# Performance work log

Hardware: AMD Instinct MI355X
Metric: run time of the kernel (lower is better)

## Reference

```python
import jax, jax.numpy as jnp
import numpy as np

B, T, D, H, L = 65536, 8, 60, 128, 64


def _lstm_layer(x, Wih, Whh, bih, bhh):
    """Single LSTM layer, batch_first. x: [B,T,Din]. Returns (ys [B,T,H], h_last [B,H]).
    PyTorch gate order: i, f, g, o."""
    Bsz = x.shape[0]
    Hd = Whh.shape[1]
    # Precompute input contribution for all timesteps: [B,T,4H]
    xg = jnp.einsum('btd,gd->btg', x, Wih) + bih + bhh

    def step(carry, xt):
        h, c = carry
        g = xt + h @ Whh.T  # [B,4H]
        i, f, gg, o = jnp.split(g, 4, axis=-1)
        i = jax.nn.sigmoid(i)
        f = jax.nn.sigmoid(f)
        gg = jnp.tanh(gg)
        o = jax.nn.sigmoid(o)
        c = f * c + i * gg
        h = o * jnp.tanh(c)
        return (h, c), h

    h0 = jnp.zeros((Bsz, Hd), x.dtype)
    c0 = jnp.zeros((Bsz, Hd), x.dtype)
    (h_last, _), ys = jax.lax.scan(step, (h0, c0), jnp.swapaxes(xg, 0, 1))
    return jnp.swapaxes(ys, 0, 1), h_last


def setup_inputs() -> dict:
    key = jax.random.key(0)
    ks = jax.random.split(key, 24)
    s = 1.0 / np.sqrt(H)  # torch LSTM/Linear default uniform bound

    def u(k, shape):
        return jax.random.uniform(k, shape, jnp.float32, -s, s)

    inp = {"x": jax.random.normal(ks[0], (B, T, D), jnp.float32)}
    # encoder layer 0 (in=D), layer 1 (in=H); decoder layer 0 (in=L), layer 1 (in=H)
    dims = {"enc0": D, "enc1": H, "dec0": L, "dec1": H}
    i = 1
    for name, din in dims.items():
        inp[name + "_Wih"] = u(ks[i], (4 * H, din)); i += 1
        inp[name + "_Whh"] = u(ks[i], (4 * H, H)); i += 1
        inp[name + "_bih"] = u(ks[i], (4 * H,)); i += 1
        inp[name + "_bhh"] = u(ks[i], (4 * H,)); i += 1
    inp["W_lat"] = u(ks[i], (L, H)); i += 1
    inp["b_lat"] = u(ks[i], (L,)); i += 1
    inp["W_out"] = jax.random.uniform(ks[i], (D, H), jnp.float32, -s, s); i += 1
    inp["b_out"] = jax.random.uniform(ks[i], (D,), jnp.float32, -s, s)
    return inp


def reference(x,
              enc0_Wih, enc0_Whh, enc0_bih, enc0_bhh,
              enc1_Wih, enc1_Whh, enc1_bih, enc1_bhh,
              dec0_Wih, dec0_Whh, dec0_bih, dec0_bhh,
              dec1_Wih, dec1_Whh, dec1_bih, dec1_bhh,
              W_lat, b_lat, W_out, b_out):
    # Encoder (eval mode: inter-layer dropout is identity)
    h1, _ = _lstm_layer(x, enc0_Wih, enc0_Whh, enc0_bih, enc0_bhh)
    _, h_last = _lstm_layer(h1, enc1_Wih, enc1_Whh, enc1_bih, enc1_bhh)
    # Latent bottleneck from top-layer final hidden state
    z = h_last @ W_lat.T + b_lat  # [B,L]
    z_seq = jnp.broadcast_to(z[:, None, :], (z.shape[0], T, z.shape[1]))
    # Decoder
    d1, _ = _lstm_layer(z_seq, dec0_Wih, dec0_Whh, dec0_bih, dec0_bhh)
    d2, _ = _lstm_layer(d1, dec1_Wih, dec1_Whh, dec1_bih, dec1_bhh)
    recon = jnp.einsum('bth,dh->btd', d2, W_out) + b_out  # [B,T,D]
    return recon
```

## Files before the change

kernel.cpp:

```cpp
#include <hip/hip_runtime.h>

typedef _Float16 f16;
typedef _Float16 f16x8 __attribute__((ext_vector_type(8)));
typedef float    f32x4 __attribute__((ext_vector_type(4)));

#define MFMA16(a,b,c) __builtin_amdgcn_mfma_f32_16x16x32_f16(a,b,c,0,0,0)

#define HIST_S 1096
#define HB_S   136
#define HB_BUF 4352

__device__ __forceinline__ float sigm(float v){
  return __builtin_amdgcn_rcpf(1.f + __builtin_amdgcn_exp2f(-1.4426950408889634f*v));
}
__device__ __forceinline__ float tanha(float v){
  return 1.f - 2.f*__builtin_amdgcn_rcpf(1.f + __builtin_amdgcn_exp2f(2.8853900817779268f*v));
}
__device__ __forceinline__ f32x4 splat4(float v){ f32x4 r; r[0]=v;r[1]=v;r[2]=v;r[3]=v; return r; }

__device__ __forceinline__ f16x8 ldfrag(const float* __restrict__ W, int K, int n, int k0){
  const float* p = W + n*K + k0;
  f32x4 a = *(const f32x4*)p;
  f32x4 b = *(const f32x4*)(p+4);
  f16x8 r;
  #pragma unroll
  for (int i=0;i<4;i++){ r[i] = (f16)a[i]; r[4+i] = (f16)b[i]; }
  return r;
}
__device__ __forceinline__ f16x8 ldfrag60(const float* __restrict__ W, int n, int k0){
  const float* p = W + n*60 + k0;
  f32x4 a = *(const f32x4*)p;
  f16x8 r;
  #pragma unroll
  for (int i=0;i<4;i++) r[i] = (f16)a[i];
  if (k0 < 56){
    f32x4 b = *(const f32x4*)(p+4);
    #pragma unroll
    for (int i=0;i<4;i++) r[4+i] = (f16)b[i];
  } else {
    #pragma unroll
    for (int i=0;i<4;i++) r[4+i] = (f16)0.f;
  }
  return r;
}
__device__ __forceinline__ f16x8 zfrag(){
  f16x8 r;
  #pragma unroll
  for (int i=0;i<8;i++) r[i] = (f16)0.f;
  return r;
}

__device__ __forceinline__ void act_update(f32x4 acc[2][4], f32x4* cst, f16* dst, int stride, int col, int qd){
  #pragma unroll
  for (int m=0;m<2;m++){
    #pragma unroll
    for (int r=0;r<4;r++){
      float ii = sigm(acc[m][0][r]);
      float ff = sigm(acc[m][1][r]);
      float gg = tanha(acc[m][2][r]);
      float oo = sigm(acc[m][3][r]);
      float cn = ff*cst[m][r] + ii*gg;
      cst[m][r] = cn;
      dst[(m*16+qd*4+r)*stride + col] = (f16)(oo*tanha(cn));
    }
  }
}

__global__ void __launch_bounds__(512, 2)
lstm_main(const float* __restrict__ x,
          const float* __restrict__ e0Wih, const float* __restrict__ e0Whh, const float* __restrict__ e0bi, const float* __restrict__ e0bh,
          const float* __restrict__ e1Wih, const float* __restrict__ e1Whh, const float* __restrict__ e1bi, const float* __restrict__ e1bh,
          const float* __restrict__ d0Wih, const float* __restrict__ d0Whh, const float* __restrict__ d0bi, const float* __restrict__ d0bh,
          const float* __restrict__ d1Wih, const float* __restrict__ d1Whh, const float* __restrict__ d1bi, const float* __restrict__ d1bh,
          const float* __restrict__ Wlat,  const float* __restrict__ blat,
          const float* __restrict__ Wout,  const float* __restrict__ bout,
          float* __restrict__ out)
{
  __shared__ __align__(16) f16 hist[32*HIST_S];
  __shared__ __align__(16) f16 hb1 [2*HB_BUF];

  const int tid = threadIdx.x;
  const int w   = tid >> 6;
  const int ln  = tid & 15;
  const int qd  = (tid >> 4) & 3;
  const int bs  = blockIdx.x << 5;
  const int col = w*16 + ln;

  f16x8 Bf[4][8];
  f32x4 acc[2][4];
  f32x4 cst[2];
  float bg[4];

  #pragma unroll
  for (int g=0;g<4;g++){
    const int n = g*128 + col;
    #pragma unroll
    for (int kb=0;kb<2;kb++) Bf[g][kb]   = ldfrag60(e0Wih, n, kb*32 + qd*8);
    #pragma unroll
    for (int kb=0;kb<4;kb++) Bf[g][kb+2] = ldfrag(e0Whh, 128, n, kb*32 + qd*8);
    bg[g] = e0bi[n] + e0bh[n];
  }
  cst[0] = splat4(0.f); cst[1] = splat4(0.f);
  for (int t=0; t<8; t++){
    #pragma unroll
    for (int m=0;m<2;m++)
      #pragma unroll
      for (int g=0;g<4;g++) acc[m][g] = splat4(bg[g]);
    #pragma unroll
    for (int kb=0; kb<2; kb++){
      #pragma unroll
      for (int m=0;m<2;m++){
        const float* p = x + (bs + m*16 + ln)*480 + t*60 + kb*32 + qd*8;
        f16x8 a;
        {
          f32x4 lo = *(const f32x4*)p;
          #pragma unroll
          for (int i=0;i<4;i++) a[i] = (f16)lo[i];
          if (kb==1 && qd==3){
            #pragma unroll
            for (int i=0;i<4;i++) a[4+i] = (f16)0.f;
          } else {
            f32x4 hi = *(const f32x4*)(p+4);
            #pragma unroll
            for (int i=0;i<4;i++) a[4+i] = (f16)hi[i];
          }
        }
        #pragma unroll
        for (int g=0; g<4; g++) acc[m][g] = MFMA16(a, Bf[g][kb], acc[m][g]);
      }
    }
    if (t > 0){
      #pragma unroll
      for (int kb=0; kb<4; kb++){
        #pragma unroll
        for (int m=0;m<2;m++){
          f16x8 a = *(const f16x8*)(hist + (m*16+ln)*HIST_S + (t-1)*HB_S + kb*32 + qd*8);
          #pragma unroll
          for (int g=0; g<4; g++) acc[m][g] = MFMA16(a, Bf[g][kb+2], acc[m][g]);
        }
      }
    }
    act_update(acc, cst, hist + t*HB_S, HIST_S, col, qd);
    __syncthreads();
  }

  #pragma unroll
  for (int g=0;g<4;g++){
    const int n = g*128 + col;
    #pragma unroll
    for (int kb=0;kb<4;kb++){
      Bf[g][kb]   = ldfrag(e1Wih, 128, n, kb*32 + qd*8);
      Bf[g][kb+4] = ldfrag(e1Whh, 128, n, kb*32 + qd*8);
    }
    bg[g] = e1bi[n] + e1bh[n];
  }
  cst[0] = splat4(0.f); cst[1] = splat4(0.f);
  for (int t=0; t<8; t++){
    #pragma unroll
    for (int m=0;m<2;m++)
      #pragma unroll
      for (int g=0;g<4;g++) acc[m][g] = splat4(bg[g]);
    #pragma unroll
    for (int kb=0; kb<4; kb++){
      #pragma unroll
      for (int m=0;m<2;m++){
        f16x8 a = *(const f16x8*)(hist + (m*16+ln)*HIST_S + t*HB_S + kb*32 + qd*8);
        #pragma unroll
        for (int g=0; g<4; g++) acc[m][g] = MFMA16(a, Bf[g][kb], acc[m][g]);
      }
    }
    if (t > 0){
      const f16* hb = hb1 + ((t-1)&1)*HB_BUF;
      #pragma unroll
      for (int kb=0; kb<4; kb++){
        #pragma unroll
        for (int m=0;m<2;m++){
          f16x8 a = *(const f16x8*)(hb + (m*16+ln)*HB_S + kb*32 + qd*8);
          #pragma unroll
          for (int g=0; g<4; g++) acc[m][g] = MFMA16(a, Bf[g][kb+4], acc[m][g]);
        }
      }
    }
    act_update(acc, cst, hb1 + (t&1)*HB_BUF, HB_S, col, qd);
    __syncthreads();
  }

  {
    const int mo = w & 1, no = w >> 1;
    const int zn = no*16 + ln;
    f32x4 zacc = splat4(blat[zn]);
    f16x8 Bz[4];
    #pragma unroll
    for (int kb=0;kb<4;kb++) Bz[kb] = ldfrag(Wlat, 128, zn, kb*32 + qd*8);
    const f16* hb = hb1 + HB_BUF;
    #pragma unroll
    for (int kb=0;kb<4;kb++){
      f16x8 a = *(const f16x8*)(hb + (mo*16+ln)*HB_S + kb*32 + qd*8);
      zacc = MFMA16(a, Bz[kb], zacc);
    }
    #pragma unroll
    for (int r=0;r<4;r++)
      hb1[(mo*16+qd*4+r)*HB_S + zn] = (f16)zacc[r];
  }
  __syncthreads();

  f32x4 xga[2][4];
  {
    f16x8 Bd[4][2];
    #pragma unroll
    for (int g=0;g<4;g++){
      const int n = g*128 + col;
      #pragma unroll
      for (int kb=0;kb<2;kb++) Bd[g][kb] = ldfrag(d0Wih, 64, n, kb*32 + qd*8);
      float bgd = d0bi[n] + d0bh[n];
      xga[0][g] = splat4(bgd); xga[1][g] = splat4(bgd);
    }
    #pragma unroll
    for (int kb=0; kb<2; kb++){
      #pragma unroll
      for (int m=0;m<2;m++){
        f16x8 a = *(const f16x8*)(hb1 + (m*16+ln)*HB_S + kb*32 + qd*8);
        #pragma unroll
        for (int g=0; g<4; g++) xga[m][g] = MFMA16(a, Bd[g][kb], xga[m][g]);
      }
    }
  }

  #pragma unroll
  for (int g=0;g<4;g++){
    const int n = g*128 + col;
    #pragma unroll
    for (int kb=0;kb<4;kb++) Bf[g][kb] = ldfrag(d0Whh, 128, n, kb*32 + qd*8);
  }
  cst[0] = splat4(0.f); cst[1] = splat4(0.f);
  for (int t=0; t<8; t++){
    #pragma unroll
    for (int m=0;m<2;m++)
      #pragma unroll
      for (int g=0;g<4;g++) acc[m][g] = xga[m][g];
    if (t > 0){
      #pragma unroll
      for (int kb=0; kb<4; kb++){
        #pragma unroll
        for (int m=0;m<2;m++){
          f16x8 a = *(const f16x8*)(hist + (m*16+ln)*HIST_S + (t-1)*HB_S + kb*32 + qd*8);
          #pragma unroll
          for (int g=0; g<4; g++) acc[m][g] = MFMA16(a, Bf[g][kb], acc[m][g]);
        }
      }
    }
    act_update(acc, cst, hist + t*HB_S, HIST_S, col, qd);
    __syncthreads();
  }

  #pragma unroll
  for (int g=0;g<4;g++){
    const int n = g*128 + col;
    #pragma unroll
    for (int kb=0;kb<4;kb++){
      Bf[g][kb]   = ldfrag(d1Wih, 128, n, kb*32 + qd*8);
      Bf[g][kb+4] = ldfrag(d1Whh, 128, n, kb*32 + qd*8);
    }
    bg[g] = d1bi[n] + d1bh[n];
  }
  const int dcol = (w>>1)*16 + ln;
  const int mo   = w & 1;
  f16x8 BO[4];
  #pragma unroll
  for (int kb=0;kb<4;kb++)
    BO[kb] = (dcol < 60) ? ldfrag(Wout, 128, dcol, kb*32 + qd*8) : zfrag();
  const float bo = (dcol < 60) ? bout[dcol] : 0.f;
  cst[0] = splat4(0.f); cst[1] = splat4(0.f);
  for (int t=0; t<8; t++){
    #pragma unroll
    for (int m=0;m<2;m++)
      #pragma unroll
      for (int g=0;g<4;g++) acc[m][g] = splat4(bg[g]);
    #pragma unroll
    for (int kb=0; kb<4; kb++){
      #pragma unroll
      for (int m=0;m<2;m++){
        f16x8 a = *(const f16x8*)(hist + (m*16+ln)*HIST_S + t*HB_S + kb*32 + qd*8);
        #pragma unroll
        for (int g=0; g<4; g++) acc[m][g] = MFMA16(a, Bf[g][kb], acc[m][g]);
      }
    }
    if (t > 0){
      const f16* hb = hb1 + ((t-1)&1)*HB_BUF;
      #pragma unroll
      for (int kb=0; kb<4; kb++){
        #pragma unroll
        for (int m=0;m<2;m++){
          f16x8 a = *(const f16x8*)(hb + (m*16+ln)*HB_S + kb*32 + qd*8);
          #pragma unroll
          for (int g=0; g<4; g++) acc[m][g] = MFMA16(a, Bf[g][kb+4], acc[m][g]);
        }
      }
    }
    act_update(acc, cst, hb1 + (t&1)*HB_BUF, HB_S, col, qd);
    __syncthreads();
    f32x4 ao = splat4(bo);
    const f16* hb2 = hb1 + (t&1)*HB_BUF + (mo*16+ln)*HB_S + qd*8;
    #pragma unroll
    for (int kb=0; kb<4; kb++){
      f16x8 a = *(const f16x8*)(hb2 + kb*32);
      ao = MFMA16(a, BO[kb], ao);
    }
    if (dcol < 60){
      #pragma unroll
      for (int r=0;r<4;r++){
        int s = mo*16 + qd*4 + r;
        out[(bs + s)*480 + t*60 + dcol] = ao[r];
      }
    }
  }
}

extern "C" void kernel_launch(void* const* d_in, const int* in_sizes, int n_in,
                              void* d_out, int out_size, void* d_ws, size_t ws_size,
                              hipStream_t stream)
{
  (void)d_ws; (void)ws_size; (void)in_sizes; (void)n_in; (void)out_size;
  hipLaunchKernelGGL(lstm_main, dim3(2048), dim3(512), 0, stream,
                     (const float*)d_in[0],
                     (const float*)d_in[1],  (const float*)d_in[2],  (const float*)d_in[3],  (const float*)d_in[4],
                     (const float*)d_in[5],  (const float*)d_in[6],  (const float*)d_in[7],  (const float*)d_in[8],
                     (const float*)d_in[9],  (const float*)d_in[10], (const float*)d_in[11], (const float*)d_in[12],
                     (const float*)d_in[13], (const float*)d_in[14], (const float*)d_in[15], (const float*)d_in[16],
                     (const float*)d_in[17], (const float*)d_in[18],
                     (const float*)d_in[19], (const float*)d_in[20],
                     (float*)d_out);
}
```

Measured before the change: 1.226 ms.

## Software-pipeline input projection of next timestep across LSTM recurrences

Each LSTM layer now computes the input-to-hidden MFMA contribution for timestep t+1 into a separate accumulator while step t's recurrent MFMAs and activations run, and loops are fully unrolled. This takes the input projection off the serial recurrent critical path so the MFMAs can overlap with activation math and the barrier. The decoder's first layer now recomputes the constant z projection every step instead of once. The extra accumulator registers may hurt occupancy.

```diff
diff --git a/kernel.cpp b/kernel.cpp
--- a/kernel.cpp
+++ b/kernel.cpp
@@ -87,10 +87,27 @@
   const int col = w*16 + ln;
 
   f16x8 Bf[4][8];
-  f32x4 acc[2][4];
+  f32x4 acc[2][4], accN[2][4];
   f32x4 cst[2];
   float bg[4];
 
+  auto xfrag = [&](int m, int t, int kb)->f16x8 {
+    const float* p = x + (bs + m*16 + ln)*480 + t*60 + kb*32 + qd*8;
+    f16x8 a;
+    f32x4 lo = *(const f32x4*)p;
+    #pragma unroll
+    for (int i=0;i<4;i++) a[i] = (f16)lo[i];
+    if (kb==1 && qd==3){
+      #pragma unroll
+      for (int i=0;i<4;i++) a[4+i] = (f16)0.f;
+    } else {
+      f32x4 hi = *(const f32x4*)(p+4);
+      #pragma unroll
+      for (int i=0;i<4;i++) a[4+i] = (f16)hi[i];
+    }
+    return a;
+  };
+
   #pragma unroll
   for (int g=0;g<4;g++){
     const int n = g*128 + col;
@@ -101,44 +118,47 @@
     bg[g] = e0bi[n] + e0bh[n];
   }
   cst[0] = splat4(0.f); cst[1] = splat4(0.f);
+  #pragma unroll
+  for (int m=0;m<2;m++)
+    #pragma unroll
+    for (int g=0;g<4;g++) accN[m][g] = splat4(bg[g]);
+  #pragma unroll
+  for (int kb=0; kb<2; kb++)
+    #pragma unroll
+    for (int m=0;m<2;m++){
+      f16x8 a = xfrag(m, 0, kb);
+      #pragma unroll
+      for (int g=0; g<4; g++) accN[m][g] = MFMA16(a, Bf[g][kb], accN[m][g]);
+    }
+  #pragma unroll
   for (int t=0; t<8; t++){
     #pragma unroll
     for (int m=0;m<2;m++)
       #pragma unroll
-      for (int g=0;g<4;g++) acc[m][g] = splat4(bg[g]);
-    #pragma unroll
-    for (int kb=0; kb<2; kb++){
-      #pragma unroll
-      for (int m=0;m<2;m++){
-        const float* p = x + (bs + m*16 + ln)*480 + t*60 + kb*32 + qd*8;
-        f16x8 a;
-        {
-          f32x4 lo = *(const f32x4*)p;
-          #pragma unroll
-          for (int i=0;i<4;i++) a[i] = (f16)lo[i];
-          if (kb==1 && qd==3){
-            #pragma unroll
-            for (int i=0;i<4;i++) a[4+i] = (f16)0.f;
-          } else {
-            f32x4 hi = *(const f32x4*)(p+4);
-            #pragma unroll
-            for (int i=0;i<4;i++) a[4+i] = (f16)hi[i];
-          }
-        }
-        #pragma unroll
-        for (int g=0; g<4; g++) acc[m][g] = MFMA16(a, Bf[g][kb], acc[m][g]);
-      }
-    }
+      for (int g=0;g<4;g++) acc[m][g] = accN[m][g];
     if (t > 0){
       #pragma unroll
-      for (int kb=0; kb<4; kb++){
+      for (int kb=0; kb<4; kb++)
         #pragma unroll
         for (int m=0;m<2;m++){
           f16x8 a = *(const f16x8*)(hist + (m*16+ln)*HIST_S + (t-1)*HB_S + kb*32 + qd*8);
           #pragma unroll
           for (int g=0; g<4; g++) acc[m][g] = MFMA16(a, Bf[g][kb+2], acc[m][g]);
         }
-      }
+    }
+    if (t < 7){
+      #pragma unroll
+      for (int m=0;m<2;m++)
+        #pragma unroll
+        for (int g=0;g<4;g++) accN[m][g] = splat4(bg[g]);
+      #pragma unroll
+      for (int kb=0; kb<2; kb++)
+        #pragma unroll
+        for (int m=0;m<2;m++){
+          f16x8 a = xfrag(m, t+1, kb);
+          #pragma unroll
+          for (int g=0; g<4; g++) accN[m][g] = MFMA16(a, Bf[g][kb], accN[m][g]);
+        }
     }
     act_update(acc, cst, hist + t*HB_S, HIST_S, col, qd);
     __syncthreads();
@@ -155,31 +175,48 @@
     bg[g] = e1bi[n] + e1bh[n];
   }
   cst[0] = splat4(0.f); cst[1] = splat4(0.f);
+  #pragma unroll
+  for (int m=0;m<2;m++)
+    #pragma unroll
+    for (int g=0;g<4;g++) accN[m][g] = splat4(bg[g]);
+  #pragma unroll
+  for (int kb=0; kb<4; kb++)
+    #pragma unroll
+    for (int m=0;m<2;m++){
+      f16x8 a = *(const f16x8*)(hist + (m*16+ln)*HIST_S + 0*HB_S + kb*32 + qd*8);
+      #pragma unroll
+      for (int g=0; g<4; g++) accN[m][g] = MFMA16(a, Bf[g][kb], accN[m][g]);
+    }
+  #pragma unroll
   for (int t=0; t<8; t++){
     #pragma unroll
     for (int m=0;m<2;m++)
       #pragma unroll
-      for (int g=0;g<4;g++) acc[m][g] = splat4(bg[g]);
-    #pragma unroll
-    for (int kb=0; kb<4; kb++){
-      #pragma unroll
-      for (int m=0;m<2;m++){
-        f16x8 a = *(const f16x8*)(hist + (m*16+ln)*HIST_S + t*HB_S + kb*32 + qd*8);
-        #pragma unroll
-        for (int g=0; g<4; g++) acc[m][g] = MFMA16(a, Bf[g][kb], acc[m][g]);
-      }
-    }
+      for (int g=0;g<4;g++) acc[m][g] = accN[m][g];
     if (t > 0){
       const f16* hb = hb1 + ((t-1)&1)*HB_BUF;
       #pragma unroll
-      for (int kb=0; kb<4; kb++){
+      for (int kb=0; kb<4; kb++)
         #pragma unroll
         for (int m=0;m<2;m++){
           f16x8 a = *(const f16x8*)(hb + (m*16+ln)*HB_S + kb*32 + qd*8);
           #pragma unroll
           for (int g=0; g<4; g++) acc[m][g] = MFMA16(a, Bf[g][kb+4], acc[m][g]);
         }
-      }
+    }
+    if (t < 7){
+      #pragma unroll
+      for (int m=0;m<2;m++)
+        #pragma unroll
+        for (int g=0;g<4;g++) accN[m][g] = splat4(bg[g]);
+      #pragma unroll
+      for (int kb=0; kb<4; kb++)
+        #pragma unroll
+        for (int m=0;m<2;m++){
+          f16x8 a = *(const f16x8*)(hist + (m*16+ln)*HIST_S + (t+1)*HB_S + kb*32 + qd*8);
+          #pragma unroll
+          for (int g=0; g<4; g++) accN[m][g] = MFMA16(a, Bf[g][kb], accN[m][g]);
+        }
     }
     act_update(acc, cst, hb1 + (t&1)*HB_BUF, HB_S, col, qd);
     __syncthreads();
@@ -204,50 +241,57 @@
   }
   __syncthreads();
 
-  f32x4 xga[2][4];
-  {
-    f16x8 Bd[4][2];
-    #pragma unroll
-    for (int g=0;g<4;g++){
-      const int n = g*128 + col;
-      #pragma unroll
-      for (int kb=0;kb<2;kb++) Bd[g][kb] = ldfrag(d0Wih, 64, n, kb*32 + qd*8);
-      float bgd = d0bi[n] + d0bh[n];
-      xga[0][g] = splat4(bgd); xga[1][g] = splat4(bgd);
-    }
-    #pragma unroll
-    for (int kb=0; kb<2; kb++){
-      #pragma unroll
-      for (int m=0;m<2;m++){
-        f16x8 a = *(const f16x8*)(hb1 + (m*16+ln)*HB_S + kb*32 + qd*8);
-        #pragma unroll
-        for (int g=0; g<4; g++) xga[m][g] = MFMA16(a, Bd[g][kb], xga[m][g]);
-      }
-    }
-  }
-
   #pragma unroll
   for (int g=0;g<4;g++){
     const int n = g*128 + col;
     #pragma unroll
-    for (int kb=0;kb<4;kb++) Bf[g][kb] = ldfrag(d0Whh, 128, n, kb*32 + qd*8);
+    for (int kb=0;kb<2;kb++) Bf[g][kb]   = ldfrag(d0Wih, 64, n, kb*32 + qd*8);
+    #pragma unroll
+    for (int kb=0;kb<4;kb++) Bf[g][kb+2] = ldfrag(d0Whh, 128, n, kb*32 + qd*8);
+    bg[g] = d0bi[n] + d0bh[n];
   }
   cst[0] = splat4(0.f); cst[1] = splat4(0.f);
+  #pragma unroll
+  for (int m=0;m<2;m++)
+    #pragma unroll
+    for (int g=0;g<4;g++) accN[m][g] = splat4(bg[g]);
+  #pragma unroll
+  for (int kb=0; kb<2; kb++)
+    #pragma unroll
+    for (int m=0;m<2;m++){
+      f16x8 a = *(const f16x8*)(hb1 + (m*16+ln)*HB_S + kb*32 + qd*8);
+      #pragma unroll
+      for (int g=0; g<4; g++) accN[m][g] = MFMA16(a, Bf[g][kb], accN[m][g]);
+    }
+  #pragma unroll
   for (int t=0; t<8; t++){
     #pragma unroll
     for (int m=0;m<2;m++)
       #pragma unroll
-      for (int g=0;g<4;g++) acc[m][g] = xga[m][g];
+      for (int g=0;g<4;g++) acc[m][g] = accN[m][g];
     if (t > 0){
       #pragma unroll
-      for (int kb=0; kb<4; kb++){
+      for (int kb=0; kb<4; kb++)
         #pragma unroll
         for (int m=0;m<2;m++){
           f16x8 a = *(const f16x8*)(hist + (m*16+ln)*HIST_S + (t-1)*HB_S + kb*32 + qd*8);
           #pragma unroll
-          for (int g=0; g<4; g++) acc[m][g] = MFMA16(a, Bf[g][kb], acc[m][g]);
-        }
-      }
+          for (int g=0; g<4; g++) acc[m][g] = MFMA16(a, Bf[g][kb+2], acc[m][g]);
+        }
+    }
+    if (t < 7){
+      #pragma unroll
+      for (int m=0;m<2;m++)
+        #pragma unroll
+        for (int g=0;g<4;g++) accN[m][g] = splat4(bg[g]);
+      #pragma unroll
+      for (int kb=0; kb<2; kb++)
+        #pragma unroll
+        for (int m=0;m<2;m++){
+          f16x8 a = *(const f16x8*)(hb1 + (m*16+ln)*HB_S + kb*32 + qd*8);
+          #pragma unroll
+          for (int g=0; g<4; g++) accN[m][g] = MFMA16(a, Bf[g][kb], accN[m][g]);
+        }
     }
     act_update(acc, cst, hist + t*HB_S, HIST_S, col, qd);
     __syncthreads();
@@ -271,31 +315,48 @@
     BO[kb] = (dcol < 60) ? ldfrag(Wout, 128, dcol, kb*32 + qd*8) : zfrag();
   const float bo = (dcol < 60) ? bout[dcol] : 0.f;
   cst[0] = splat4(0.f); cst[1] = splat4(0.f);
+  #pragma unroll
+  for (int m=0;m<2;m++)
+    #pragma unroll
+    for (int g=0;g<4;g++) accN[m][g] = splat4(bg[g]);
+  #pragma unroll
+  for (int kb=0; kb<4; kb++)
+    #pragma unroll
+    for (int m=0;m<2;m++){
+      f16x8 a = *(const f16x8*)(hist + (m*16+ln)*HIST_S + 0*HB_S + kb*32 + qd*8);
+      #pragma unroll
+      for (int g=0; g<4; g++) accN[m][g] = MFMA16(a, Bf[g][kb], accN[m][g]);
+    }
+  #pragma unroll
   for (int t=0; t<8; t++){
     #pragma unroll
     for (int m=0;m<2;m++)
       #pragma unroll
-      for (int g=0;g<4;g++) acc[m][g] = splat4(bg[g]);
-    #pragma unroll
-    for (int kb=0; kb<4; kb++){
-      #pragma unroll
-      for (int m=0;m<2;m++){
-        f16x8 a = *(const f16x8*)(hist + (m*16+ln)*HIST_S + t*HB_S + kb*32 + qd*8);
-        #pragma unroll
-        for (int g=0; g<4; g++) acc[m][g] = MFMA16(a, Bf[g][kb], acc[m][g]);
-      }
-    }
+      for (int g=0;g<4;g++) acc[m][g] = accN[m][g];
     if (t > 0){
       const f16* hb = hb1 + ((t-1)&1)*HB_BUF;
       #pragma unroll
-      for (int kb=0; kb<4; kb++){
+      for (int kb=0; kb<4; kb++)
         #pragma unroll
         for (int m=0;m<2;m++){
           f16x8 a = *(const f16x8*)(hb + (m*16+ln)*HB_S + kb*32 + qd*8);
           #pragma unroll
           for (int g=0; g<4; g++) acc[m][g] = MFMA16(a, Bf[g][kb+4], acc[m][g]);
         }
-      }
+    }
+    if (t < 7){
+      #pragma unroll
+      for (int m=0;m<2;m++)
+        #pragma unroll
+        for (int g=0;g<4;g++) accN[m][g] = splat4(bg[g]);
+      #pragma unroll
+      for (int kb=0; kb<4; kb++)
+        #pragma unroll
+        for (int m=0;m<2;m++){
+          f16x8 a = *(const f16x8*)(hist + (m*16+ln)*HIST_S + (t+1)*HB_S + kb*32 + qd*8);
+          #pragma unroll
+          for (int g=0; g<4; g++) accN[m][g] = MFMA16(a, Bf[g][kb], accN[m][g]);
+        }
     }
     act_update(acc, cst, hb1 + (t&1)*HB_BUF, HB_S, col, qd);
     __syncthreads();
```

After: 1.371 ms. 11.8% more time.
